# Optimization experiments

Hardware: AMD Instinct MI355X
Metric: run time of the kernel (lower is better)

Reference implementation:

```python
import jax, jax.numpy as jnp
import numpy as np

N_OBJ, N_ROOM, N_ATTR = 20000, 500, 2000
IN_FEATS, H = 300, 512
E_OO, E_RO, E_AO = 640000, 50000, 100000
B = 8


def setup_inputs() -> dict:
    key = jax.random.key(0)
    ks = jax.random.split(key, 16)
    s = 0.05
    inp = {
        'frames': jax.random.normal(ks[0], (B, H), jnp.float32),
        'feat_object': jax.random.normal(ks[1], (N_OBJ, IN_FEATS), jnp.float32),
        'feat_room': jax.random.normal(ks[2], (N_ROOM, IN_FEATS), jnp.float32),
        'feat_attr': jax.random.normal(ks[3], (N_ATTR, IN_FEATS), jnp.float32),
        'W1_interacts': jax.random.normal(ks[4], (IN_FEATS, H), jnp.float32) * s,
        'b1_interacts': jnp.zeros((H,), jnp.float32),
        'W1_behave': jax.random.normal(ks[5], (IN_FEATS, H), jnp.float32) * s,
        'b1_behave': jnp.zeros((H,), jnp.float32),
        'W2_interacts': jax.random.normal(ks[6], (H, H), jnp.float32) * s,
        'b2_interacts': jnp.zeros((H,), jnp.float32),
        'src_oo': jax.random.randint(ks[7], (E_OO,), 0, N_OBJ, jnp.int32),
        'dst_oo': jax.random.randint(ks[8], (E_OO,), 0, N_OBJ, jnp.int32),
        'src_ro': jax.random.randint(ks[9], (E_RO,), 0, N_ROOM, jnp.int32),
        'dst_ro': jax.random.randint(ks[10], (E_RO,), 0, N_OBJ, jnp.int32),
        'src_ao': jax.random.randint(ks[11], (E_AO,), 0, N_ATTR, jnp.int32),
        'dst_ao': jax.random.randint(ks[12], (E_AO,), 0, N_OBJ, jnp.int32),
    }
    return inp


def _graph_conv(feat_src, src, dst, n_dst, W, b, relu):
    # DGL GraphConv, norm='both': D_dst^{-1/2} A D_src^{-1/2} X W + b
    n_src = feat_src.shape[0]
    ones_e = jnp.ones(src.shape[0], feat_src.dtype)
    deg_out = jax.ops.segment_sum(ones_e, src, num_segments=n_src)
    norm_src = jnp.clip(deg_out, 1.0, None) ** -0.5
    msg = (feat_src * norm_src[:, None])[src]          # [E, F] gather
    agg = jax.ops.segment_sum(msg, dst, num_segments=n_dst)  # scatter-sum
    deg_in = jax.ops.segment_sum(ones_e, dst, num_segments=n_dst)
    norm_dst = jnp.clip(deg_in, 1.0, None) ** -0.5
    out = (agg * norm_dst[:, None]) @ W + b
    return jax.nn.relu(out) if relu else out


def reference(frames, feat_object, feat_room, feat_attr,
              W1_interacts, b1_interacts, W1_behave, b1_behave,
              W2_interacts, b2_interacts,
              src_oo, dst_oo, src_ro, dst_ro, src_ao, dst_ao):
    # conv1: three relations, all dst='object'; HeteroGraphConv mean aggregate
    h_oo = _graph_conv(feat_object, src_oo, dst_oo, N_OBJ, W1_interacts, b1_interacts, True)
    h_ro = _graph_conv(feat_room, src_ro, dst_ro, N_OBJ, W1_interacts, b1_interacts, True)
    h_ao = _graph_conv(feat_attr, src_ao, dst_ao, N_OBJ, W1_behave, b1_behave, True)
    h_obj = (h_oo + h_ro + h_ao) / 3.0
    # conv2: only object->object (room not in conv1 output dict); mean over 1 rel
    h2 = _graph_conv(h_obj, src_oo, dst_oo, N_OBJ, W2_interacts, b2_interacts, False)
    # HETAttention=True: repeat over frames batch dim
    x = jnp.broadcast_to(h2[None], (frames.shape[0], N_OBJ, H))
    return x
```

## Files before the change

kernel.cpp:

```cpp
#include <hip/hip_runtime.h>

#define N_OBJ  20000
#define N_ROOM 500
#define N_ATTR 2000
#define IN_F   300
#define HDIM   512
#define E_OO   640000
#define E_RO   50000
#define E_AO   100000
#define BATCH  8

typedef __attribute__((ext_vector_type(8))) __bf16 bf16x8;
typedef __attribute__((ext_vector_type(4))) float  f32x4;

__device__ inline unsigned short f2bf_rn(float x)
{
    unsigned u = __float_as_uint(x);
    unsigned r = (u + 0x7fffu + ((u >> 16) & 1u)) >> 16;
    return (unsigned short)r;
}
__device__ inline float bf2f(unsigned short h)
{
    return __uint_as_float(((unsigned)h) << 16);
}

__global__ void count_edges(const int* __restrict__ src_oo, const int* __restrict__ dst_oo,
                            const int* __restrict__ src_ro, const int* __restrict__ dst_ro,
                            const int* __restrict__ src_ao, const int* __restrict__ dst_ao,
                            int* cnt_src_oo, int* cnt_src_ro, int* cnt_src_ao,
                            int* cnt_dst_oo, int* cnt_dst_ro, int* cnt_dst_ao)
{
    int e = blockIdx.x * blockDim.x + threadIdx.x;
    const int total = E_OO + E_RO + E_AO;
    if (e >= total) return;
    if (e < E_OO) {
        atomicAdd(&cnt_src_oo[src_oo[e]], 1);
        atomicAdd(&cnt_dst_oo[dst_oo[e]], 1);
    } else if (e < E_OO + E_RO) {
        int i = e - E_OO;
        atomicAdd(&cnt_src_ro[src_ro[i]], 1);
        atomicAdd(&cnt_dst_ro[dst_ro[i]], 1);
    } else {
        int i = e - E_OO - E_RO;
        atomicAdd(&cnt_src_ao[src_ao[i]], 1);
        atomicAdd(&cnt_dst_ao[dst_ao[i]], 1);
    }
}

__global__ __launch_bounds__(1024)
void scan3(const int* c0, const int* c1, const int* c2,
           int* r0, int* r1, int* r2,
           int* u0, int* u1, int* u2)
{
    const int n = N_OBJ;
    const int* cnt = (blockIdx.x == 0) ? c0 : (blockIdx.x == 1 ? c1 : c2);
    int* rp  = (blockIdx.x == 0) ? r0 : (blockIdx.x == 1 ? r1 : r2);
    int* cur = (blockIdx.x == 0) ? u0 : (blockIdx.x == 1 ? u1 : u2);

    __shared__ int part[1024];
    int t  = threadIdx.x;
    int lo = t * 20;
    int hi = lo + 20 < n ? lo + 20 : n;

    int local = 0;
    for (int i = lo; i < hi; ++i) local += cnt[i];
    part[t] = local;
    __syncthreads();
    for (int off = 1; off < 1024; off <<= 1) {
        int v = (t >= off) ? part[t - off] : 0;
        __syncthreads();
        part[t] += v;
        __syncthreads();
    }
    int run = part[t] - local;
    for (int i = lo; i < hi; ++i) {
        rp[i]  = run;
        cur[i] = run;
        run += cnt[i];
    }
    if (t == 1023) rp[n] = part[1023];
}

__global__ void norms6(const int* c0, const int* c1, const int* c2,
                       const int* c3, const int* c4, const int* c5,
                       float* n0, float* n1, float* n2,
                       float* n3, float* n4, float* n5,
                       int s0, int s1, int s2, int s3, int s4, int s5)
{
    const int* c; float* o; int n;
    switch (blockIdx.y) {
        case 0:  c = c0; o = n0; n = s0; break;
        case 1:  c = c1; o = n1; n = s1; break;
        case 2:  c = c2; o = n2; n = s2; break;
        case 3:  c = c3; o = n3; n = s3; break;
        case 4:  c = c4; o = n4; n = s4; break;
        default: c = c5; o = n5; n = s5; break;
    }
    int i = blockIdx.x * blockDim.x + threadIdx.x;
    if (i < n) {
        int d = c[i];
        if (d < 1) d = 1;
        o[i] = 1.0f / sqrtf((float)d);
    }
}

__global__ void fill_edges(const int* __restrict__ src_oo, const int* __restrict__ dst_oo,
                           const int* __restrict__ src_ro, const int* __restrict__ dst_ro,
                           const int* __restrict__ src_ao, const int* __restrict__ dst_ao,
                           int* cur_oo, int* cur_ro, int* cur_ao,
                           int* col_oo, int* col_ro, int* col_ao)
{
    int e = blockIdx.x * blockDim.x + threadIdx.x;
    const int total = E_OO + E_RO + E_AO;
    if (e >= total) return;
    if (e < E_OO) {
        int pos = atomicAdd(&cur_oo[dst_oo[e]], 1);
        col_oo[pos] = src_oo[e];
    } else if (e < E_OO + E_RO) {
        int i = e - E_OO;
        int pos = atomicAdd(&cur_ro[dst_ro[i]], 1);
        col_ro[pos] = src_ro[i];
    } else {
        int i = e - E_OO - E_RO;
        int pos = atomicAdd(&cur_ao[dst_ao[i]], 1);
        col_ao[pos] = src_ao[i];
    }
}

__global__ void pack_w(const float* __restrict__ W, int K, int Kp,
                       unsigned short* __restrict__ Wp)
{
    int Keff = 3 * Kp;
    int idx = blockIdx.x * 256 + threadIdx.x;
    if (idx >= HDIM * Keff) return;
    int n  = idx / Keff;
    int kp = idx - n * Keff;
    int term = (kp >= 2 * Kp) ? 2 : (kp >= Kp ? 1 : 0);
    int ks = kp - term * Kp;
    float v = (ks < K) ? W[(size_t)ks * HDIM + n] : 0.0f;
    unsigned short h = f2bf_rn(v);
    unsigned short out = (term == 1) ? f2bf_rn(v - bf2f(h)) : h;
    Wp[idx] = out;
}

__global__ __launch_bounds__(256)
void agg_csr_split(const float* __restrict__ feat, int F, int Fp,
                   const int* __restrict__ rp, const int* __restrict__ col,
                   const float* __restrict__ nsrc, const float* __restrict__ ndst,
                   float scale,
                   unsigned short* __restrict__ hi, unsigned short* __restrict__ lo)
{
    int d = blockIdx.x;
    int t = threadIdx.x;
    int a = rp[d], b = rp[d + 1];
    int f2 = 256 + t;
    bool has2  = (f2 < Fp);
    bool real2 = (f2 < F);
    float acc0 = 0.f, acc1 = 0.f;
    for (int j = a; j < b; ++j) {
        int s = col[j];
        float ns = nsrc[s] * scale;
        acc0 += feat[(size_t)s * F + t] * ns;
        if (real2) acc1 += feat[(size_t)s * F + f2] * ns;
    }
    float nd = ndst[d];
    acc0 *= nd;
    acc1 = real2 ? acc1 * nd : 0.f;

    size_t o0 = (size_t)d * Fp + t;
    unsigned short h0 = f2bf_rn(acc0);
    hi[o0] = h0;
    lo[o0] = f2bf_rn(acc0 - bf2f(h0));
    if (has2) {
        size_t o1 = (size_t)d * Fp + f2;
        unsigned short h1 = f2bf_rn(acc1);
        hi[o1] = h1;
        lo[o1] = f2bf_rn(acc1 - bf2f(h1));
    }
}

template<int EPI>
__global__ __launch_bounds__(256)
void gemm_mfma(const unsigned short* __restrict__ Ah,
               const unsigned short* __restrict__ Al,
               const unsigned short* __restrict__ Wp,
               const float* __restrict__ bias,
               float* __restrict__ C,
               int M, int Kp)
{
    const int LDT = 40;
    __shared__ unsigned short As[128 * LDT];
    __shared__ unsigned short Bs[128 * LDT];

    int tid  = threadIdx.x;
    int lane = tid & 63;
    int wave = tid >> 6;
    int wm = (wave & 1) * 64;
    int wn = (wave >> 1) * 64;
    int m0 = blockIdx.x * 128;
    int n0 = blockIdx.y * 128;
    int Keff = 3 * Kp;
    int rw = lane & 15;
    int q  = lane >> 4;

    f32x4 acc[4][4];
#pragma unroll
    for (int i = 0; i < 4; ++i)
#pragma unroll
        for (int j = 0; j < 4; ++j) acc[i][j] = (f32x4)0.0f;

    for (int k0 = 0; k0 < Keff; k0 += 32) {
        int term = (k0 >= 2 * Kp) ? 2 : (k0 >= Kp ? 1 : 0);
        int kb = k0 - ((term == 2) ? 2 * Kp : (term == 1 ? Kp : 0));
        const unsigned short* Asrc = (term == 2) ? Al : Ah;
#pragma unroll
        for (int h = 0; h < 2; ++h) {
            int idx = tid + h * 256;
            int m = idx >> 2, kc = (idx & 3) * 8;
            int gm = m0 + m;
            uint4 v = make_uint4(0u, 0u, 0u, 0u);
            if (gm < M) v = *(const uint4*)(Asrc + (size_t)gm * Kp + kb + kc);
            *(uint4*)&As[m * LDT + kc] = v;
        }
#pragma unroll
        for (int h = 0; h < 2; ++h) {
            int idx = tid + h * 256;
            int nn = idx >> 2, kc = (idx & 3) * 8;
            uint4 v = *(const uint4*)(Wp + (size_t)(n0 + nn) * Keff + k0 + kc);
            *(uint4*)&Bs[nn * LDT + kc] = v;
        }
        __syncthreads();

        bf16x8 af[4], bfr[4];
#pragma unroll
        for (int i = 0; i < 4; ++i) {
            af[i]  = __builtin_bit_cast(bf16x8, *(const uint4*)&As[(wm + i * 16 + rw) * LDT + q * 8]);
            bfr[i] = __builtin_bit_cast(bf16x8, *(const uint4*)&Bs[(wn + i * 16 + rw) * LDT + q * 8]);
        }
#pragma unroll
        for (int i = 0; i < 4; ++i)
#pragma unroll
            for (int j = 0; j < 4; ++j)
                acc[i][j] = __builtin_amdgcn_mfma_f32_16x16x32_bf16(af[i], bfr[j], acc[i][j], 0, 0, 0);
        __syncthreads();
    }

    const size_t slice = (size_t)N_OBJ * HDIM;
#pragma unroll
    for (int j = 0; j < 4; ++j) {
        int n = n0 + wn + j * 16 + rw;
        float bv = bias[n];
#pragma unroll
        for (int i = 0; i < 4; ++i) {
#pragma unroll
            for (int r = 0; r < 4; ++r) {
                int m = m0 + wm + i * 16 + q * 4 + r;
                if (m < M) {
                    float v = acc[i][j][r] + bv;
                    size_t o = (size_t)m * HDIM + n;
                    if (EPI == 0)      C[o] = fmaxf(v, 0.f);
                    else if (EPI == 1) C[o] += fmaxf(v, 0.f);
                    else if (EPI == 2) {
#pragma unroll
                        for (int c = 0; c < BATCH; ++c) C[c * slice + o] = v;
                    } else             C[o] = v;
                }
            }
        }
    }
}

__global__ void bcast8(const float4* __restrict__ src, float4* __restrict__ dst)
{
    const long long slice4 = (long long)N_OBJ * HDIM / 4;
    long long i = (long long)blockIdx.x * blockDim.x + threadIdx.x;
    float4 v = src[i];
#pragma unroll
    for (int c = 1; c < BATCH; ++c)
        dst[c * slice4 + i] = v;
}

extern "C" void kernel_launch(void* const* d_in, const int* in_sizes, int n_in,
                              void* d_out, int out_size, void* d_ws, size_t ws_size,
                              hipStream_t stream)
{
    const float* feat_object = (const float*)d_in[1];
    const float* feat_room   = (const float*)d_in[2];
    const float* feat_attr   = (const float*)d_in[3];
    const float* W1i = (const float*)d_in[4];
    const float* b1i = (const float*)d_in[5];
    const float* W1b = (const float*)d_in[6];
    const float* b1b = (const float*)d_in[7];
    const float* W2  = (const float*)d_in[8];
    const float* b2  = (const float*)d_in[9];
    const int* src_oo = (const int*)d_in[10];
    const int* dst_oo = (const int*)d_in[11];
    const int* src_ro = (const int*)d_in[12];
    const int* dst_ro = (const int*)d_in[13];
    const int* src_ao = (const int*)d_in[14];
    const int* dst_ao = (const int*)d_in[15];
    float* out = (float*)d_out;

    const size_t slice = (size_t)N_OBJ * HDIM;
    const int KP1 = 320;
    const int KP2 = 512;

    const size_t NEED = 130u * 1024u * 1024u;
    bool use_ws = (ws_size >= NEED);
    char* base = use_ws ? (char*)d_ws : (char*)(out + slice);
    size_t off = 0;
    auto alloc = [&](size_t bytes) -> void* {
        void* p = base + off;
        off += (bytes + 255) & ~(size_t)255;
        return p;
    };

    float* n_src_oo = (float*)alloc(N_OBJ  * 4);
    float* n_src_ro = (float*)alloc(N_ROOM * 4);
    float* n_src_ao = (float*)alloc(N_ATTR * 4);
    float* n_dst_oo = (float*)alloc(N_OBJ * 4);
    float* n_dst_ro = (float*)alloc(N_OBJ * 4);
    float* n_dst_ao = (float*)alloc(N_OBJ * 4);

    const int CNT_TOTAL = N_OBJ + 512 + 2048 + 3 * N_OBJ;
    int* cnt_blk    = (int*)alloc((size_t)CNT_TOTAL * 4);
    int* cnt_src_oo = cnt_blk;
    int* cnt_src_ro = cnt_src_oo + N_OBJ;
    int* cnt_src_ao = cnt_src_ro + 512;
    int* cnt_dst_oo = cnt_src_ao + 2048;
    int* cnt_dst_ro = cnt_dst_oo + N_OBJ;
    int* cnt_dst_ao = cnt_dst_ro + N_OBJ;

    int* rp_oo  = (int*)alloc((N_OBJ + 1) * 4);
    int* rp_ro  = (int*)alloc((N_OBJ + 1) * 4);
    int* rp_ao  = (int*)alloc((N_OBJ + 1) * 4);
    int* cur_oo = (int*)alloc(N_OBJ * 4);
    int* cur_ro = (int*)alloc(N_OBJ * 4);
    int* cur_ao = (int*)alloc(N_OBJ * 4);
    int* col_oo = (int*)alloc((size_t)E_OO * 4);
    int* col_ro = (int*)alloc((size_t)E_RO * 4);
    int* col_ao = (int*)alloc((size_t)E_AO * 4);

    unsigned short* Ah1 = (unsigned short*)alloc((size_t)N_OBJ * KP1 * 2);
    unsigned short* Al1 = (unsigned short*)alloc((size_t)N_OBJ * KP1 * 2);
    unsigned short* Ah2 = (unsigned short*)alloc((size_t)N_OBJ * KP2 * 2);
    unsigned short* Al2 = (unsigned short*)alloc((size_t)N_OBJ * KP2 * 2);
    unsigned short* Wp1i = (unsigned short*)alloc((size_t)HDIM * 3 * KP1 * 2);
    unsigned short* Wp1b = (unsigned short*)alloc((size_t)HDIM * 3 * KP1 * 2);
    unsigned short* Wp2  = (unsigned short*)alloc((size_t)HDIM * 3 * KP2 * 2);
    float* h_sum = (float*)alloc(slice * 4);

    hipMemsetAsync(cnt_blk, 0, (size_t)CNT_TOTAL * 4, stream);
    const int TOTAL_E = E_OO + E_RO + E_AO;
    int egrid = (TOTAL_E + 255) / 256;
    count_edges<<<egrid, 256, 0, stream>>>(src_oo, dst_oo, src_ro, dst_ro, src_ao, dst_ao,
                                           cnt_src_oo, cnt_src_ro, cnt_src_ao,
                                           cnt_dst_oo, cnt_dst_ro, cnt_dst_ao);
    scan3<<<3, 1024, 0, stream>>>(cnt_dst_oo, cnt_dst_ro, cnt_dst_ao,
                                  rp_oo, rp_ro, rp_ao, cur_oo, cur_ro, cur_ao);
    norms6<<<dim3((N_OBJ + 255) / 256, 6), 256, 0, stream>>>(
        cnt_src_oo, cnt_src_ro, cnt_src_ao, cnt_dst_oo, cnt_dst_ro, cnt_dst_ao,
        n_src_oo, n_src_ro, n_src_ao, n_dst_oo, n_dst_ro, n_dst_ao,
        N_OBJ, N_ROOM, N_ATTR, N_OBJ, N_OBJ, N_OBJ);
    fill_edges<<<egrid, 256, 0, stream>>>(src_oo, dst_oo, src_ro, dst_ro, src_ao, dst_ao,
                                          cur_oo, cur_ro, cur_ao, col_oo, col_ro, col_ao);

    {
        int e1 = HDIM * 3 * KP1, e2 = HDIM * 3 * KP2;
        pack_w<<<(e1 + 255) / 256, 256, 0, stream>>>(W1i, IN_F, KP1, Wp1i);
        pack_w<<<(e1 + 255) / 256, 256, 0, stream>>>(W1b, IN_F, KP1, Wp1b);
        pack_w<<<(e2 + 255) / 256, 256, 0, stream>>>(W2, HDIM, KP2, Wp2);
    }

    dim3 ggrid((N_OBJ + 127) / 128, HDIM / 128);

    agg_csr_split<<<N_OBJ, 256, 0, stream>>>(feat_object, IN_F, KP1, rp_oo, col_oo,
                                             n_src_oo, n_dst_oo, 1.0f, Ah1, Al1);
    gemm_mfma<0><<<ggrid, 256, 0, stream>>>(Ah1, Al1, Wp1i, b1i, h_sum, N_OBJ, KP1);

    agg_csr_split<<<N_OBJ, 256, 0, stream>>>(feat_room, IN_F, KP1, rp_ro, col_ro,
                                             n_src_ro, n_dst_ro, 1.0f, Ah1, Al1);
    gemm_mfma<1><<<ggrid, 256, 0, stream>>>(Ah1, Al1, Wp1i, b1i, h_sum, N_OBJ, KP1);

    agg_csr_split<<<N_OBJ, 256, 0, stream>>>(feat_attr, IN_F, KP1, rp_ao, col_ao,
                                             n_src_ao, n_dst_ao, 1.0f, Ah1, Al1);
    gemm_mfma<1><<<ggrid, 256, 0, stream>>>(Ah1, Al1, Wp1b, b1b, h_sum, N_OBJ, KP1);

    agg_csr_split<<<N_OBJ, 256, 0, stream>>>(h_sum, HDIM, KP2, rp_oo, col_oo,
                                             n_src_oo, n_dst_oo, 1.0f / 3.0f, Ah2, Al2);
    if (use_ws) {
        gemm_mfma<2><<<ggrid, 256, 0, stream>>>(Ah2, Al2, Wp2, b2, out, N_OBJ, KP2);
    } else {
        gemm_mfma<3><<<ggrid, 256, 0, stream>>>(Ah2, Al2, Wp2, b2, out, N_OBJ, KP2);
        const long long slice4 = (long long)slice / 4;
        bcast8<<<(unsigned)(slice4 / 256), 256, 0, stream>>>((const float4*)out, (float4*)out);
    }
}
```

Baseline: 1.182 ms.

## Chunk CSR aggregation per wave and use direct global-to-LDS loads with XCD remap

Replaces the one-block-per-node aggregation with a 128-thread kernel where each wave handles one destination node and one of eight feature chunks. It also prefetches the next neighbour's feature and norm before accumulating, which is meant to hide gather latency and raise parallelism. The MFMA GEMM now stages A/B tiles with global_load_lds 16-byte loads instead of register round-trips and drops the LDS row padding, which may add bank conflicts. It remaps a 1D grid so consecutive tiles land on the same XCD for cache reuse. The M-bound check on A loads is removed, so it reads past row 20000 unless the buffers are padded.

```diff
diff --git a/kernel.cpp b/kernel.cpp
--- a/kernel.cpp
+++ b/kernel.cpp
@@ -22,6 +22,14 @@
 __device__ inline float bf2f(unsigned short h)
 {
     return __uint_as_float(((unsigned)h) << 16);
+}
+
+__device__ inline void gload16(const unsigned short* g, unsigned short* l)
+{
+    __builtin_amdgcn_global_load_lds(
+        (const __attribute__((address_space(1))) void*)g,
+        (__attribute__((address_space(3))) void*)l,
+        16, 0, 0);
 }
 
 __global__ void count_edges(const int* __restrict__ src_oo, const int* __restrict__ dst_oo,
@@ -143,39 +151,44 @@
     Wp[idx] = out;
 }
 
-__global__ __launch_bounds__(256)
-void agg_csr_split(const float* __restrict__ feat, int F, int Fp,
-                   const int* __restrict__ rp, const int* __restrict__ col,
-                   const float* __restrict__ nsrc, const float* __restrict__ ndst,
-                   float scale,
-                   unsigned short* __restrict__ hi, unsigned short* __restrict__ lo)
-{
-    int d = blockIdx.x;
-    int t = threadIdx.x;
+__global__ __launch_bounds__(128)
+void agg_chunk(const float* __restrict__ feat, int F, int Fp, int CW,
+               const int* __restrict__ rp, const int* __restrict__ col,
+               const float* __restrict__ nsrc, const float* __restrict__ ndst,
+               float scale,
+               unsigned short* __restrict__ hi, unsigned short* __restrict__ lo)
+{
+    int c0 = (blockIdx.x & 7) * CW;
+    int d  = ((blockIdx.x >> 3) << 1) + (threadIdx.x >> 6);
+    int t  = threadIdx.x & 63;
+    int cc = c0 + t;
+    bool act  = (t < CW);
+    bool real = act && (cc < F);
+
     int a = rp[d], b = rp[d + 1];
-    int f2 = 256 + t;
-    bool has2  = (f2 < Fp);
-    bool real2 = (f2 < F);
-    float acc0 = 0.f, acc1 = 0.f;
-    for (int j = a; j < b; ++j) {
-        int s = col[j];
-        float ns = nsrc[s] * scale;
-        acc0 += feat[(size_t)s * F + t] * ns;
-        if (real2) acc1 += feat[(size_t)s * F + f2] * ns;
-    }
-    float nd = ndst[d];
-    acc0 *= nd;
-    acc1 = real2 ? acc1 * nd : 0.f;
-
-    size_t o0 = (size_t)d * Fp + t;
-    unsigned short h0 = f2bf_rn(acc0);
-    hi[o0] = h0;
-    lo[o0] = f2bf_rn(acc0 - bf2f(h0));
-    if (has2) {
-        size_t o1 = (size_t)d * Fp + f2;
-        unsigned short h1 = f2bf_rn(acc1);
-        hi[o1] = h1;
-        lo[o1] = f2bf_rn(acc1 - bf2f(h1));
+    int n = b - a;
+    float acc = 0.f;
+
+    int   s_nx = (n > 0) ? col[a] : 0;
+    float f_nx = (real && n > 0) ? feat[(size_t)s_nx * F + cc] : 0.f;
+    float w_nx = (n > 0) ? nsrc[s_nx] * scale : 0.f;
+    for (int i = 0; i < n; ++i) {
+        float fc = f_nx, wc = w_nx;
+        int i1 = i + 1;
+        if (i1 < n) {
+            int s1 = col[a + i1];
+            f_nx = real ? feat[(size_t)s1 * F + cc] : 0.f;
+            w_nx = nsrc[s1] * scale;
+        }
+        acc += fc * wc;
+    }
+
+    if (act) {
+        float v = real ? acc * ndst[d] : 0.f;
+        size_t o = (size_t)d * Fp + cc;
+        unsigned short h = f2bf_rn(v);
+        hi[o] = h;
+        lo[o] = f2bf_rn(v - bf2f(h));
     }
 }
 
@@ -186,22 +199,29 @@
                const unsigned short* __restrict__ Wp,
                const float* __restrict__ bias,
                float* __restrict__ C,
-               int M, int Kp)
-{
-    const int LDT = 40;
-    __shared__ unsigned short As[128 * LDT];
-    __shared__ unsigned short Bs[128 * LDT];
+               int M, int Kp, int nwg)
+{
+    __shared__ unsigned short As[128 * 32];
+    __shared__ unsigned short Bs[128 * 32];
+
+    int orig = blockIdx.x;
+    int qq8 = nwg >> 3, r8 = nwg & 7, xcd = orig & 7;
+    int w = (xcd < r8 ? xcd * (qq8 + 1) : r8 * (qq8 + 1) + (xcd - r8) * qq8) + (orig >> 3);
+    int m0 = (w >> 2) * 128;
+    int n0 = (w & 3) * 128;
 
     int tid  = threadIdx.x;
     int lane = tid & 63;
     int wave = tid >> 6;
     int wm = (wave & 1) * 64;
     int wn = (wave >> 1) * 64;
-    int m0 = blockIdx.x * 128;
-    int n0 = blockIdx.y * 128;
     int Keff = 3 * Kp;
     int rw = lane & 15;
     int q  = lane >> 4;
+
+    int rb  = wave * 32;
+    int rl  = lane >> 2;
+    int klo = (lane & 3) * 8;
 
     f32x4 acc[4][4];
 #pragma unroll
@@ -213,29 +233,18 @@
         int term = (k0 >= 2 * Kp) ? 2 : (k0 >= Kp ? 1 : 0);
         int kb = k0 - ((term == 2) ? 2 * Kp : (term == 1 ? Kp : 0));
         const unsigned short* Asrc = (term == 2) ? Al : Ah;
-#pragma unroll
-        for (int h = 0; h < 2; ++h) {
-            int idx = tid + h * 256;
-            int m = idx >> 2, kc = (idx & 3) * 8;
-            int gm = m0 + m;
-            uint4 v = make_uint4(0u, 0u, 0u, 0u);
-            if (gm < M) v = *(const uint4*)(Asrc + (size_t)gm * Kp + kb + kc);
-            *(uint4*)&As[m * LDT + kc] = v;
-        }
-#pragma unroll
-        for (int h = 0; h < 2; ++h) {
-            int idx = tid + h * 256;
-            int nn = idx >> 2, kc = (idx & 3) * 8;
-            uint4 v = *(const uint4*)(Wp + (size_t)(n0 + nn) * Keff + k0 + kc);
-            *(uint4*)&Bs[nn * LDT + kc] = v;
-        }
+
+        gload16(Asrc + (size_t)(m0 + rb + rl) * Kp + kb + klo,        &As[rb * 32]);
+        gload16(Asrc + (size_t)(m0 + rb + 16 + rl) * Kp + kb + klo,   &As[(rb + 16) * 32]);
+        gload16(Wp   + (size_t)(n0 + rb + rl) * Keff + k0 + klo,      &Bs[rb * 32]);
+        gload16(Wp   + (size_t)(n0 + rb + 16 + rl) * Keff + k0 + klo, &Bs[(rb + 16) * 32]);
         __syncthreads();
 
         bf16x8 af[4], bfr[4];
 #pragma unroll
         for (int i = 0; i < 4; ++i) {
-            af[i]  = __builtin_bit_cast(bf16x8, *(const uint4*)&As[(wm + i * 16 + rw) * LDT + q * 8]);
-            bfr[i] = __builtin_bit_cast(bf16x8, *(const uint4*)&Bs[(wn + i * 16 + rw) * LDT + q * 8]);
+            af[i]  = __builtin_bit_cast(bf16x8, *(const uint4*)&As[(wm + i * 16 + rw) * 32 + q * 8]);
+            bfr[i] = __builtin_bit_cast(bf16x8, *(const uint4*)&Bs[(wn + i * 16 + rw) * 32 + q * 8]);
         }
 #pragma unroll
         for (int i = 0; i < 4; ++i)
@@ -372,26 +381,28 @@
         pack_w<<<(e2 + 255) / 256, 256, 0, stream>>>(W2, HDIM, KP2, Wp2);
     }
 
-    dim3 ggrid((N_OBJ + 127) / 128, HDIM / 128);
-
-    agg_csr_split<<<N_OBJ, 256, 0, stream>>>(feat_object, IN_F, KP1, rp_oo, col_oo,
-                                             n_src_oo, n_dst_oo, 1.0f, Ah1, Al1);
-    gemm_mfma<0><<<ggrid, 256, 0, stream>>>(Ah1, Al1, Wp1i, b1i, h_sum, N_OBJ, KP1);
-
-    agg_csr_split<<<N_OBJ, 256, 0, stream>>>(feat_room, IN_F, KP1, rp_ro, col_ro,
-                                             n_src_ro, n_dst_ro, 1.0f, Ah1, Al1);
-    gemm_mfma<1><<<ggrid, 256, 0, stream>>>(Ah1, Al1, Wp1i, b1i, h_sum, N_OBJ, KP1);
-
-    agg_csr_split<<<N_OBJ, 256, 0, stream>>>(feat_attr, IN_F, KP1, rp_ao, col_ao,
-                                             n_src_ao, n_dst_ao, 1.0f, Ah1, Al1);
-    gemm_mfma<1><<<ggrid, 256, 0, stream>>>(Ah1, Al1, Wp1b, b1b, h_sum, N_OBJ, KP1);
-
-    agg_csr_split<<<N_OBJ, 256, 0, stream>>>(h_sum, HDIM, KP2, rp_oo, col_oo,
-                                             n_src_oo, n_dst_oo, 1.0f / 3.0f, Ah2, Al2);
+    const int AGG_GRID = (N_OBJ / 2) * 8;
+    int mt = (N_OBJ + 127) / 128;
+    int nwg = mt * 4;
+
+    agg_chunk<<<AGG_GRID, 128, 0, stream>>>(feat_object, IN_F, KP1, KP1 / 8, rp_oo, col_oo,
+                                            n_src_oo, n_dst_oo, 1.0f, Ah1, Al1);
+    gemm_mfma<0><<<nwg, 256, 0, stream>>>(Ah1, Al1, Wp1i, b1i, h_sum, N_OBJ, KP1, nwg);
+
+    agg_chunk<<<AGG_GRID, 128, 0, stream>>>(feat_room, IN_F, KP1, KP1 / 8, rp_ro, col_ro,
+                                            n_src_ro, n_dst_ro, 1.0f, Ah1, Al1);
+    gemm_mfma<1><<<nwg, 256, 0, stream>>>(Ah1, Al1, Wp1i, b1i, h_sum, N_OBJ, KP1, nwg);
+
+    agg_chunk<<<AGG_GRID, 128, 0, stream>>>(feat_attr, IN_F, KP1, KP1 / 8, rp_ao, col_ao,
+                                            n_src_ao, n_dst_ao, 1.0f, Ah1, Al1);
+    gemm_mfma<1><<<nwg, 256, 0, stream>>>(Ah1, Al1, Wp1b, b1b, h_sum, N_OBJ, KP1, nwg);
+
+    agg_chunk<<<AGG_GRID, 128, 0, stream>>>(h_sum, HDIM, KP2, KP2 / 8, rp_oo, col_oo,
+                                            n_src_oo, n_dst_oo, 1.0f / 3.0f, Ah2, Al2);
     if (use_ws) {
-        gemm_mfma<2><<<ggrid, 256, 0, stream>>>(Ah2, Al2, Wp2, b2, out, N_OBJ, KP2);
+        gemm_mfma<2><<<nwg, 256, 0, stream>>>(Ah2, Al2, Wp2, b2, out, N_OBJ, KP2, nwg);
     } else {
-        gemm_mfma<3><<<ggrid, 256, 0, stream>>>(Ah2, Al2, Wp2, b2, out, N_OBJ, KP2);
+        gemm_mfma<3><<<nwg, 256, 0, stream>>>(Ah2, Al2, Wp2, b2, out, N_OBJ, KP2, nwg);
         const long long slice4 = (long long)slice / 4;
         bcast8<<<(unsigned)(slice4 / 256), 256, 0, stream>>>((const float4*)out, (float4*)out);
     }
```

Result: slower. 1.801 ms (+52.4%).
